# Kernel optimization log

Measured on AMD Instinct MI355X. Metric: run time of the kernel, lower is better.

The kernel has to match this reference:

```python
import jax, jax.numpy as jnp
import numpy as np

LN_EPS = 1e-12  # BERT LayerNorm eps


def _layernorm(x, g, b):
    mu = jnp.mean(x, axis=-1, keepdims=True)
    var = jnp.mean(jnp.square(x - mu), axis=-1, keepdims=True)
    return (x - mu) * jax.lax.rsqrt(var + LN_EPS) * g + b


def setup_inputs() -> dict:
    key = jax.random.key(0)
    B, M, D, H, dh, R, Ro, Rf, F = 4, 2048, 768, 12, 64, 32, 256, 256, 3072
    ks = iter(jax.random.split(key, 32))
    n = lambda shape, s=0.02: jax.random.normal(next(ks), shape, jnp.float32) * s
    return {
        'x': jax.random.normal(next(ks), (B, M, D), jnp.float32),
        'mask': jnp.zeros((B, M), jnp.float32),  # HF-style additive mask
        'Pq': n((H, D, R)), 'Vq': n((H, R, dh)), 'bq': n((1, H, 1, dh)),
        'Pk': n((H, D, R)), 'Vk': n((H, R, dh)), 'bk': n((1, H, 1, dh)),
        'Pv': n((H, D, R)), 'Vv': n((H, R, dh)), 'bv': n((1, H, 1, dh)),
        'Uo': n((D, Ro)), 'Vo': n((Ro, D)), 'bo_attn': jnp.zeros((D,), jnp.float32),
        'U1': n((D, Rf)), 'V1': n((Rf, F)), 'b1': jnp.zeros((F,), jnp.float32),
        'U2': n((F, Rf)), 'V2': n((Rf, D)), 'b2': jnp.zeros((D,), jnp.float32),
        'ln1_g': jnp.ones((D,), jnp.float32), 'ln1_b': jnp.zeros((D,), jnp.float32),
        'ln2_g': jnp.ones((D,), jnp.float32), 'ln2_b': jnp.zeros((D,), jnp.float32),
    }


def reference(x, mask, Pq, Vq, bq, Pk, Vk, bk, Pv, Vv, bv,
              Uo, Vo, bo_attn, U1, V1, b1, U2, V2, b2,
              ln1_g, ln1_b, ln2_g, ln2_b):
    B, M, D = x.shape
    H, dh = Pq.shape[0], Vq.shape[2]
    # low-rank per-head Q/K/V: x @ P (bhmr) then @ V (bhmd) + bias
    q = jnp.einsum('bhmr,hrd->bhmd', jnp.einsum('bmd,hdr->bhmr', x, Pq), Vq) + bq
    k = jnp.einsum('bhmr,hrd->bhmd', jnp.einsum('bmd,hdr->bhmr', x, Pk), Vk) + bk
    v = jnp.einsum('bhmr,hrd->bhmd', jnp.einsum('bmd,hdr->bhmr', x, Pv), Vv) + bv
    # attention (flash_svd_attention math: scaled dot-product + additive mask)
    scores = jnp.einsum('bhmd,bhnd->bhmn', q, k) / jnp.sqrt(jnp.float32(dh))
    scores = scores + mask[:, None, None, :]
    attn = jnp.einsum('bhmn,bhnd->bhmd', jax.nn.softmax(scores, axis=-1), v)
    attn = attn.transpose(0, 2, 1, 3).reshape(B, M, D)
    # low-rank output projection + residual + LN1
    x1 = _layernorm(x + (attn @ Uo) @ Vo + bo_attn, ln1_g, ln1_b)
    # low-rank FFN (BERT intermediate: exact GELU)
    mid = x1 @ U1
    y = (jax.nn.gelu(mid @ V1 + b1, approximate=False) @ U2) @ V2 + b2
    return _layernorm(x1 + y, ln2_g, ln2_b)
```

## Files before the change

### kernel.cpp

```cpp
#include <hip/hip_runtime.h>
#include <hip/hip_bf16.h>
#include <math.h>

typedef __hip_bfloat16 bf16;
typedef __attribute__((ext_vector_type(8))) short short8;
typedef __attribute__((ext_vector_type(4))) short short4v;
typedef __attribute__((ext_vector_type(4))) float f32x4;

__device__ __forceinline__ float to_f(float x) { return x; }
__device__ __forceinline__ float to_f(bf16 x) { return __bfloat162float(x); }

template <typename T> __device__ __forceinline__ T from_f(float x);
template <> __device__ __forceinline__ float from_f<float>(float x) { return x; }
template <> __device__ __forceinline__ bf16 from_f<bf16>(float x) { return __float2bfloat16(x); }

__device__ __forceinline__ float gelu_exact(float x) {
    return 0.5f * x * (1.0f + erff(x * 0.70710678118654752f));
}

#define GLD_LDS16(g, l)                                               \
    __builtin_amdgcn_global_load_lds(                                 \
        (const __attribute__((address_space(1))) void*)(g),           \
        (__attribute__((address_space(3))) void*)(l), 16, 0, 0)

__global__ __launch_bounds__(256) void build_w_qkv_lds(const float* __restrict__ Pq,
                                                       const float* __restrict__ Vq,
                                                       const float* __restrict__ Pk,
                                                       const float* __restrict__ Vk,
                                                       const float* __restrict__ Pv,
                                                       const float* __restrict__ Vv,
                                                       bf16* __restrict__ Wt) {
    const int dt = blockIdx.x;
    const int h = blockIdx.y;
    const int which = blockIdx.z;
    const float* P = (which == 0) ? Pq : (which == 1) ? Pk : Pv;
    const float* V = (which == 0) ? Vq : (which == 1) ? Vk : Vv;
    __shared__ __align__(16) float Ps[128][36];
    __shared__ __align__(16) float Vs[32][64];
    __shared__ __align__(16) unsigned int Ot[64][68];
    const int tid = threadIdx.x;

    const float* pbase = P + ((size_t)h * 768 + dt * 128) * 32;
#pragma unroll
    for (int i = 0; i < 4; i++) {
        int idx = tid + i * 256;
        float4 v4 = ((const float4*)pbase)[idx];
        *(float4*)&Ps[idx >> 3][(idx & 7) * 4] = v4;
    }
    const float* vbase = V + (size_t)h * 2048;
#pragma unroll
    for (int i = 0; i < 2; i++) {
        int idx = tid + i * 256;
        ((float4*)&Vs[0][0])[idx] = ((const float4*)vbase)[idx];
    }
    __syncthreads();

    const int e = tid & 63, w = tid >> 6;
    float vreg[32];
#pragma unroll
    for (int r = 0; r < 32; r++) vreg[r] = Vs[r][e];

#pragma unroll
    for (int dp = 0; dp < 16; dp++) {
        const int d0 = w * 32 + dp * 2;
        float a0 = 0.f, a1 = 0.f;
#pragma unroll
        for (int r4 = 0; r4 < 8; r4++) {
            float4 p0 = *(const float4*)&Ps[d0][r4 * 4];
            float4 p1 = *(const float4*)&Ps[d0 + 1][r4 * 4];
            a0 += p0.x * vreg[r4 * 4] + p0.y * vreg[r4 * 4 + 1] + p0.z * vreg[r4 * 4 + 2] + p0.w * vreg[r4 * 4 + 3];
            a1 += p1.x * vreg[r4 * 4] + p1.y * vreg[r4 * 4 + 1] + p1.z * vreg[r4 * 4 + 2] + p1.w * vreg[r4 * 4 + 3];
        }
        unsigned int lo = (unsigned int)(unsigned short)__builtin_bit_cast(short, from_f<bf16>(a0));
        unsigned int hi = (unsigned int)(unsigned short)__builtin_bit_cast(short, from_f<bf16>(a1));
        Ot[e][w * 16 + dp] = lo | (hi << 16);
    }
    __syncthreads();

    const int erow = tid >> 2, c0 = (tid & 3) * 16;
    bf16* dst = Wt + ((size_t)which * 768 + h * 64 + erow) * 768 + dt * 128 + c0 * 2;
    uint4 u0 = *(const uint4*)&Ot[erow][c0];
    uint4 u1 = *(const uint4*)&Ot[erow][c0 + 4];
    uint4 u2 = *(const uint4*)&Ot[erow][c0 + 8];
    uint4 u3 = *(const uint4*)&Ot[erow][c0 + 12];
    *(uint4*)(dst) = u0;
    *(uint4*)(dst + 8) = u1;
    *(uint4*)(dst + 16) = u2;
    *(uint4*)(dst + 24) = u3;
}

__global__ __launch_bounds__(256) void cast_transpose_t(const float* __restrict__ in,
                                                        bf16* __restrict__ out,
                                                        int R, int Cc) {
    __shared__ float t[32][33];
    const int r0 = blockIdx.x * 32, c0 = blockIdx.y * 32;
    const int tx = threadIdx.x & 31, ty = threadIdx.x >> 5;
#pragma unroll
    for (int i = 0; i < 4; i++)
        t[ty + i * 8][tx] = in[(size_t)(r0 + ty + i * 8) * Cc + c0 + tx];
    __syncthreads();
#pragma unroll
    for (int i = 0; i < 4; i++)
        out[(size_t)(c0 + ty + i * 8) * R + r0 + tx] = from_f<bf16>(t[tx][ty + i * 8]);
}

__global__ __launch_bounds__(256) void cast_f32_bf16(const float* __restrict__ in,
                                                     bf16* __restrict__ out, int n4) {
    int t = blockIdx.x * 256 + threadIdx.x;
    if (t >= n4) return;
    float4 v = ((const float4*)in)[t];
    bf16 tmp[4] = {from_f<bf16>(v.x), from_f<bf16>(v.y), from_f<bf16>(v.z), from_f<bf16>(v.w)};
    ((short4v*)out)[t] = *(short4v*)tmp;
}

__global__ __launch_bounds__(256) void pack_bias_qkv(const float* __restrict__ bq,
                                                     const float* __restrict__ bk,
                                                     const float* __restrict__ bv,
                                                     float* __restrict__ out) {
    int t = blockIdx.x * 256 + threadIdx.x;
    if (t >= 768) return;
    out[t] = bq[t];
    out[768 + t] = bk[t];
    out[1536 + t] = bv[t];
}

template <typename TOUT, int EPI>
__global__ __launch_bounds__(256) void gemm_mfma(const bf16* __restrict__ A,
                                                 const bf16* __restrict__ Bt,
                                                 const float* __restrict__ bias,
                                                 TOUT* __restrict__ C,
                                                 int M, int N, int K) {
    __shared__ __align__(16) bf16 As[128 * 32];
    __shared__ __align__(16) bf16 Bs[128 * 32];
    const int tid = threadIdx.x;
    const int w = tid >> 6, lane = tid & 63;
    const int l = lane & 15, quad = lane >> 4;
    const int wm = w >> 1, wn = w & 1;
    const int m0 = blockIdx.x * 128, n0 = blockIdx.y * 128;

    const int r_in = lane >> 2;
    const int slot = lane & 3;
    const int rA0 = 2 * w * 16 + r_in, rA1 = rA0 + 16;
    const int q0 = slot ^ ((rA0 >> 1) & 3);
    const int q1 = slot ^ ((rA1 >> 1) & 3);
    const bf16* a0 = A + (size_t)(m0 + rA0) * K + q0 * 8;
    const bf16* a1 = A + (size_t)(m0 + rA1) * K + q1 * 8;
    const bf16* b0 = Bt + (size_t)(n0 + rA0) * K + q0 * 8;
    const bf16* b1 = Bt + (size_t)(n0 + rA1) * K + q1 * 8;
    bf16* lA0 = As + 2 * w * 512;
    bf16* lA1 = lA0 + 512;
    bf16* lB0 = Bs + 2 * w * 512;
    bf16* lB1 = lB0 + 512;

    const int swz = (quad ^ ((l >> 1) & 3)) * 8;
    f32x4 acc[4][4] = {};

    for (int k0 = 0; k0 < K; k0 += 32) {
        GLD_LDS16(a0 + k0, lA0);
        GLD_LDS16(a1 + k0, lA1);
        GLD_LDS16(b0 + k0, lB0);
        GLD_LDS16(b1 + k0, lB1);
        __syncthreads();
        short8 af[4], bfr[4];
#pragma unroll
        for (int mt = 0; mt < 4; mt++)
            af[mt] = *(const short8*)&As[(wm * 64 + mt * 16 + l) * 32 + swz];
#pragma unroll
        for (int nt = 0; nt < 4; nt++)
            bfr[nt] = *(const short8*)&Bs[(wn * 64 + nt * 16 + l) * 32 + swz];
#pragma unroll
        for (int mt = 0; mt < 4; mt++)
#pragma unroll
            for (int nt = 0; nt < 4; nt++)
                acc[mt][nt] = __builtin_amdgcn_mfma_f32_16x16x32_bf16(af[mt], bfr[nt], acc[mt][nt], 0, 0, 0);
        __syncthreads();
    }

    float bs[4];
#pragma unroll
    for (int nt = 0; nt < 4; nt++)
        bs[nt] = bias ? bias[n0 + wn * 64 + nt * 16 + l] : 0.f;
#pragma unroll
    for (int mt = 0; mt < 4; mt++) {
#pragma unroll
        for (int nt = 0; nt < 4; nt++) {
            const int col = n0 + wn * 64 + nt * 16 + l;
#pragma unroll
            for (int r = 0; r < 4; r++) {
                const int row = m0 + wm * 64 + mt * 16 + quad * 4 + r;
                float val = acc[mt][nt][r] + bs[nt];
                if (EPI == 1) val = gelu_exact(val);
                C[(size_t)row * N + col] = from_f<TOUT>(val);
            }
        }
    }
}

__global__ __launch_bounds__(256) void transpose_v(const bf16* __restrict__ qkv,
                                                   bf16* __restrict__ vt) {
    __shared__ __align__(16) bf16 t[64][72];
    const int m0 = blockIdx.x * 64;
    const int h = blockIdx.y;
    const int tid = threadIdx.x;
    const int r = tid >> 2, c0 = (tid & 3) * 16;
    {
        const size_t g = (size_t)(m0 + r) * 2304 + 1536 + h * 64 + c0;
        *(short8*)&t[r][c0] = *(const short8*)(qkv + g);
        *(short8*)&t[r][c0 + 8] = *(const short8*)(qkv + g + 8);
    }
    __syncthreads();
    const int b = m0 >> 11, mm = m0 & 2047;
    const int e = tid >> 2, mi0 = (tid & 3) * 16;
    bf16 tmp[16];
#pragma unroll
    for (int j = 0; j < 16; j++) tmp[j] = t[mi0 + j][e];
    bf16* dst = vt + (((size_t)b * 12 + h) * 64 + e) * 2048 + mm + mi0;
    *(short8*)dst = *(short8*)&tmp[0];
    *(short8*)(dst + 8) = *(short8*)&tmp[8];
}

__global__ __launch_bounds__(256, 2) void flash_attn_mfma(const bf16* __restrict__ qkv,
                                                          const bf16* __restrict__ vt,
                                                          const float* __restrict__ mask,
                                                          bf16* __restrict__ attn) {
    const int qt = blockIdx.x, h = blockIdx.y, b = blockIdx.z;
    const int tid = threadIdx.x;
    const int w = tid >> 6, lane = tid & 63;
    const int l = lane & 15, quad = lane >> 4;

    __shared__ __align__(16) bf16 Ks[64 * 64];
    __shared__ __align__(16) bf16 Vs[64 * 64];
    __shared__ __align__(16) bf16 Ps[4][16 * 64];
    __shared__ float msk2[64];

    const float C1 = 0.125f * 1.44269504088896f;

    short8 qf[2][2];
#pragma unroll
    for (int mt = 0; mt < 2; mt++) {
        const int qrow = qt * 128 + w * 32 + mt * 16 + l;
        const bf16* qp = qkv + ((size_t)b * 2048 + qrow) * 2304 + h * 64 + quad * 8;
        qf[mt][0] = *(const short8*)qp;
        qf[mt][1] = *(const short8*)(qp + 32);
    }

    f32x4 of[2][4] = {};
    float lsum[2] = {0.f, 0.f};

    for (int kc = 0; kc < 2048; kc += 64) {
        __syncthreads();
#pragma unroll
        for (int i = 0; i < 2; i++) {
            const int cid = (w * 2 + i) * 64 + lane;
            const int row = cid >> 3, slot = cid & 7;
            const int gq = slot ^ (row & 7);
            const bf16* kp = qkv + ((size_t)b * 2048 + kc + row) * 2304 + 768 + h * 64 + gq * 8;
            GLD_LDS16(kp, &Ks[(size_t)cid * 8]);
            const bf16* vp = vt + (((size_t)b * 12 + h) * 64 + row) * 2048 + kc + gq * 8;
            GLD_LDS16(vp, &Vs[(size_t)cid * 8]);
        }
        if (tid < 64) msk2[tid] = mask[(size_t)b * 2048 + kc + tid] * 1.44269504088896f;
        __syncthreads();

        f32x4 st[2][4];
#pragma unroll
        for (int nt = 0; nt < 4; nt++) {
            const int rb = (nt * 16 + l) * 64;
            short8 kf0 = *(const short8*)&Ks[rb + ((quad) ^ (l & 7)) * 8];
            short8 kf1 = *(const short8*)&Ks[rb + ((4 + quad) ^ (l & 7)) * 8];
#pragma unroll
            for (int mt = 0; mt < 2; mt++) {
                f32x4 a = {};
                a = __builtin_amdgcn_mfma_f32_16x16x32_bf16(kf0, qf[mt][0], a, 0, 0, 0);
                a = __builtin_amdgcn_mfma_f32_16x16x32_bf16(kf1, qf[mt][1], a, 0, 0, 0);
                st[mt][nt] = a;
            }
        }

        float mk[4][4];
#pragma unroll
        for (int nt = 0; nt < 4; nt++)
#pragma unroll
            for (int r = 0; r < 4; r++) mk[nt][r] = msk2[nt * 16 + quad * 4 + r];

#pragma unroll
        for (int mt = 0; mt < 2; mt++) {
#pragma unroll
            for (int nt = 0; nt < 4; nt++) {
                short4v ps;
#pragma unroll
                for (int r = 0; r < 4; r++) {
                    float p = exp2f(fmaf(st[mt][nt][r], C1, mk[nt][r]));
                    lsum[mt] += p;
                    ps[r] = __builtin_bit_cast(short, from_f<bf16>(p));
                }
                const int slot8 = (2 * nt + (quad >> 1)) ^ (l & 7);
                *(short4v*)&Ps[w][mt * 0 + l * 64 + slot8 * 8 + (quad & 1) * 4] = ps;
            }
            short8 pa0 = *(const short8*)&Ps[w][l * 64 + ((quad) ^ (l & 7)) * 8];
            short8 pa1 = *(const short8*)&Ps[w][l * 64 + ((4 + quad) ^ (l & 7)) * 8];
#pragma unroll
            for (int nt = 0; nt < 4; nt++) {
                const int rb = (nt * 16 + l) * 64;
                short8 vf0 = *(const short8*)&Vs[rb + ((quad) ^ (l & 7)) * 8];
                short8 vf1 = *(const short8*)&Vs[rb + ((4 + quad) ^ (l & 7)) * 8];
                of[mt][nt] = __builtin_amdgcn_mfma_f32_16x16x32_bf16(pa0, vf0, of[mt][nt], 0, 0, 0);
                of[mt][nt] = __builtin_amdgcn_mfma_f32_16x16x32_bf16(pa1, vf1, of[mt][nt], 0, 0, 0);
            }
        }
    }

#pragma unroll
    for (int mt = 0; mt < 2; mt++) {
        lsum[mt] += __shfl_xor(lsum[mt], 16, 64);
        lsum[mt] += __shfl_xor(lsum[mt], 32, 64);
        lsum[mt] = 1.f / lsum[mt];
    }
#pragma unroll
    for (int mt = 0; mt < 2; mt++) {
#pragma unroll
        for (int r = 0; r < 4; r++) {
            const float iv = __shfl(lsum[mt], (lane & 48) | (quad * 4 + r), 64);
            const int row = qt * 128 + w * 32 + mt * 16 + quad * 4 + r;
#pragma unroll
            for (int nt = 0; nt < 4; nt++)
                attn[((size_t)b * 2048 + row) * 768 + h * 64 + nt * 16 + l] =
                    from_f<bf16>(of[mt][nt][r] * iv);
        }
    }
}

template <typename TIN, typename TOUT>
__global__ __launch_bounds__(256) void ln_kernel(const TIN* __restrict__ base,
                                                 const float* __restrict__ add,
                                                 const float* __restrict__ gamma,
                                                 const float* __restrict__ beta,
                                                 TOUT* __restrict__ out) {
    const int row = blockIdx.x;
    const int tid = threadIdx.x;
    __shared__ float red[4];
    const size_t o = (size_t)row * 768;
    float v[3];
#pragma unroll
    for (int i = 0; i < 3; i++) {
        int d = tid + i * 256;
        v[i] = to_f(base[o + d]) + add[o + d];
    }
    float s = v[0] + v[1] + v[2];
#pragma unroll
    for (int off = 32; off > 0; off >>= 1) s += __shfl_down(s, off, 64);
    const int wave = tid >> 6, lane = tid & 63;
    if (lane == 0) red[wave] = s;
    __syncthreads();
    float mu = (red[0] + red[1] + red[2] + red[3]) * (1.0f / 768.0f);
    float d0 = v[0] - mu, d1 = v[1] - mu, d2 = v[2] - mu;
    float sq = d0 * d0 + d1 * d1 + d2 * d2;
    __syncthreads();
#pragma unroll
    for (int off = 32; off > 0; off >>= 1) sq += __shfl_down(sq, off, 64);
    if (lane == 0) red[wave] = sq;
    __syncthreads();
    float var = (red[0] + red[1] + red[2] + red[3]) * (1.0f / 768.0f);
    float rs = rsqrtf(var + 1e-12f);
#pragma unroll
    for (int i = 0; i < 3; i++) {
        int d = tid + i * 256;
        float y = (v[i] - mu) * rs * gamma[d] + beta[d];
        out[o + d] = from_f<TOUT>(y);
    }
}

extern "C" void kernel_launch(void* const* d_in, const int* in_sizes, int n_in,
                              void* d_out, int out_size, void* d_ws, size_t ws_size,
                              hipStream_t stream) {
    const float* x    = (const float*)d_in[0];
    const float* mask = (const float*)d_in[1];
    const float* Pq = (const float*)d_in[2];
    const float* Vq = (const float*)d_in[3];
    const float* bq = (const float*)d_in[4];
    const float* Pk = (const float*)d_in[5];
    const float* Vk = (const float*)d_in[6];
    const float* bk = (const float*)d_in[7];
    const float* Pv = (const float*)d_in[8];
    const float* Vv = (const float*)d_in[9];
    const float* bv = (const float*)d_in[10];
    const float* Uo = (const float*)d_in[11];
    const float* Vo = (const float*)d_in[12];
    const float* bo = (const float*)d_in[13];
    const float* U1 = (const float*)d_in[14];
    const float* V1 = (const float*)d_in[15];
    const float* b1 = (const float*)d_in[16];
    const float* U2 = (const float*)d_in[17];
    const float* V2 = (const float*)d_in[18];
    const float* b2 = (const float*)d_in[19];
    const float* g1 = (const float*)d_in[20];
    const float* be1 = (const float*)d_in[21];
    const float* g2 = (const float*)d_in[22];
    const float* be2 = (const float*)d_in[23];

    char* p = (char*)d_ws;
    bf16* Wqkv_t = (bf16*)p;            p += (size_t)2304 * 768 * 2;
    bf16* Wo_t   = (bf16*)p;            p += (size_t)768 * 768 * 2;
    bf16* U1t    = (bf16*)p;            p += (size_t)256 * 768 * 2;
    bf16* V1t    = (bf16*)p;            p += (size_t)3072 * 256 * 2;
    bf16* U2t    = (bf16*)p;            p += (size_t)256 * 3072 * 2;
    bf16* V2t    = (bf16*)p;            p += (size_t)768 * 256 * 2;
    float* bias_qkv = (float*)p;        p += (size_t)2304 * 4;
    bf16* xb     = (bf16*)p;
    bf16* x1b    = xb;                  p += (size_t)8192 * 768 * 2;
    bf16* qkv    = (bf16*)p;
    bf16* gbuf   = qkv;                 p += (size_t)8192 * 2304 * 2;
    bf16* vtb    = (bf16*)p;            p += (size_t)8192 * 768 * 2;
    bf16* attnb  = (bf16*)p;
    bf16* t2     = attnb;               p += (size_t)8192 * 768 * 2;
    float* bufA  = (float*)p;           p += (size_t)8192 * 768 * 4;
    bf16* t1     = (bf16*)p;            p += (size_t)8192 * 256 * 2;
    bf16* Vot = (bf16*)bufA;
    bf16* Uob = Vot + (size_t)768 * 256;

    build_w_qkv_lds<<<dim3(6, 12, 3), 256, 0, stream>>>(Pq, Vq, Pk, Vk, Pv, Vv, Wqkv_t);
    cast_transpose_t<<<dim3(8, 24), 256, 0, stream>>>(Vo, Vot, 256, 768);
    cast_f32_bf16<<<192, 256, 0, stream>>>(Uo, Uob, 768 * 256 / 4);
    gemm_mfma<bf16, 0><<<dim3(6, 6), 256, 0, stream>>>(Vot, Uob, nullptr, Wo_t, 768, 768, 256);
    cast_transpose_t<<<dim3(24, 8), 256, 0, stream>>>(U1, U1t, 768, 256);
    cast_transpose_t<<<dim3(8, 96), 256, 0, stream>>>(V1, V1t, 256, 3072);
    cast_transpose_t<<<dim3(96, 8), 256, 0, stream>>>(U2, U2t, 3072, 256);
    cast_transpose_t<<<dim3(8, 24), 256, 0, stream>>>(V2, V2t, 256, 768);
    pack_bias_qkv<<<3, 256, 0, stream>>>(bq, bk, bv, bias_qkv);
    cast_f32_bf16<<<6144, 256, 0, stream>>>(x, xb, 8192 * 768 / 4);

    gemm_mfma<bf16, 0><<<dim3(64, 18), 256, 0, stream>>>(xb, Wqkv_t, bias_qkv, qkv, 8192, 2304, 768);

    transpose_v<<<dim3(128, 12), 256, 0, stream>>>(qkv, vtb);

    flash_attn_mfma<<<dim3(16, 12, 4), 256, 0, stream>>>(qkv, vtb, mask, attnb);

    gemm_mfma<float, 0><<<dim3(64, 6), 256, 0, stream>>>(attnb, Wo_t, bo, bufA, 8192, 768, 768);

    ln_kernel<float, bf16><<<8192, 256, 0, stream>>>(x, bufA, g1, be1, x1b);

    gemm_mfma<bf16, 0><<<dim3(64, 2), 256, 0, stream>>>(x1b, U1t, nullptr, t1, 8192, 256, 768);

    gemm_mfma<bf16, 1><<<dim3(64, 24), 256, 0, stream>>>(t1, V1t, b1, gbuf, 8192, 3072, 256);

    gemm_mfma<bf16, 0><<<dim3(64, 2), 256, 0, stream>>>(gbuf, U2t, nullptr, t2, 8192, 256, 3072);

    gemm_mfma<float, 0><<<dim3(64, 6), 256, 0, stream>>>(t2, V2t, b2, bufA, 8192, 768, 256);

    ln_kernel<bf16, float><<<8192, 256, 0, stream>>>(x1b, bufA, g2, be2, (float*)d_out);
}
```

Baseline: 484.9 us.

## Switch flash attention to 32x32x16 MFMA with two 64-row waves per block

Rewrites the attention kernel to use 32x32x16 bf16 MFMA tiles instead of 16x16x32, with each of two waves owning 64 query rows (block shrinks from 256 to 128 threads). This doubles per-wave work, increasing reuse of K/V fragments loaded from LDS and cutting LDS reads per MFMA. The trade-offs are higher register pressure from the larger accumulators, fewer waves per block to hide latency, and a softmax normaliser that now round-trips through shared memory. A small cosmetic cleanup in build_w_qkv_lds is also included.

```diff
diff --git a/kernel.cpp b/kernel.cpp
--- a/kernel.cpp
+++ b/kernel.cpp
@@ -6,6 +6,7 @@
 typedef __attribute__((ext_vector_type(8))) short short8;
 typedef __attribute__((ext_vector_type(4))) short short4v;
 typedef __attribute__((ext_vector_type(4))) float f32x4;
+typedef __attribute__((ext_vector_type(16))) float f32x16;
 
 __device__ __forceinline__ float to_f(float x) { return x; }
 __device__ __forceinline__ float to_f(bf16 x) { return __bfloat162float(x); }
@@ -79,14 +80,10 @@
 
     const int erow = tid >> 2, c0 = (tid & 3) * 16;
     bf16* dst = Wt + ((size_t)which * 768 + h * 64 + erow) * 768 + dt * 128 + c0 * 2;
-    uint4 u0 = *(const uint4*)&Ot[erow][c0];
-    uint4 u1 = *(const uint4*)&Ot[erow][c0 + 4];
-    uint4 u2 = *(const uint4*)&Ot[erow][c0 + 8];
-    uint4 u3 = *(const uint4*)&Ot[erow][c0 + 12];
-    *(uint4*)(dst) = u0;
-    *(uint4*)(dst + 8) = u1;
-    *(uint4*)(dst + 16) = u2;
-    *(uint4*)(dst + 24) = u3;
+    *(uint4*)(dst) = *(const uint4*)&Ot[erow][c0];
+    *(uint4*)(dst + 8) = *(const uint4*)&Ot[erow][c0 + 4];
+    *(uint4*)(dst + 16) = *(const uint4*)&Ot[erow][c0 + 8];
+    *(uint4*)(dst + 24) = *(const uint4*)&Ot[erow][c0 + 12];
 }
 
 __global__ __launch_bounds__(256) void cast_transpose_t(const float* __restrict__ in,
@@ -219,39 +216,40 @@
     *(short8*)(dst + 8) = *(short8*)&tmp[8];
 }
 
-__global__ __launch_bounds__(256, 2) void flash_attn_mfma(const bf16* __restrict__ qkv,
+__global__ __launch_bounds__(128, 2) void flash_attn_mfma(const bf16* __restrict__ qkv,
                                                           const bf16* __restrict__ vt,
                                                           const float* __restrict__ mask,
                                                           bf16* __restrict__ attn) {
     const int qt = blockIdx.x, h = blockIdx.y, b = blockIdx.z;
     const int tid = threadIdx.x;
     const int w = tid >> 6, lane = tid & 63;
-    const int l = lane & 15, quad = lane >> 4;
+    const int l31 = lane & 31, hl = lane >> 5;
 
     __shared__ __align__(16) bf16 Ks[64 * 64];
     __shared__ __align__(16) bf16 Vs[64 * 64];
-    __shared__ __align__(16) bf16 Ps[4][16 * 64];
-    __shared__ float msk2[64];
+    __shared__ __align__(16) bf16 Ps[2][64 * 64];
+    __shared__ __align__(16) float msk2[64];
+    __shared__ float lsq[128];
 
     const float C1 = 0.125f * 1.44269504088896f;
 
-    short8 qf[2][2];
-#pragma unroll
-    for (int mt = 0; mt < 2; mt++) {
-        const int qrow = qt * 128 + w * 32 + mt * 16 + l;
-        const bf16* qp = qkv + ((size_t)b * 2048 + qrow) * 2304 + h * 64 + quad * 8;
-        qf[mt][0] = *(const short8*)qp;
-        qf[mt][1] = *(const short8*)(qp + 32);
-    }
-
-    f32x4 of[2][4] = {};
+    short8 qf[2][4];
+#pragma unroll
+    for (int nq = 0; nq < 2; nq++) {
+        const int qrow = qt * 128 + w * 64 + nq * 32 + l31;
+        const bf16* qp = qkv + ((size_t)b * 2048 + qrow) * 2304 + h * 64 + 8 * hl;
+#pragma unroll
+        for (int dep = 0; dep < 4; dep++) qf[nq][dep] = *(const short8*)(qp + dep * 16);
+    }
+
+    f32x16 of[2][2] = {};
     float lsum[2] = {0.f, 0.f};
 
     for (int kc = 0; kc < 2048; kc += 64) {
         __syncthreads();
 #pragma unroll
-        for (int i = 0; i < 2; i++) {
-            const int cid = (w * 2 + i) * 64 + lane;
+        for (int i = 0; i < 4; i++) {
+            const int cid = i * 128 + tid;
             const int row = cid >> 3, slot = cid & 7;
             const int gq = slot ^ (row & 7);
             const bf16* kp = qkv + ((size_t)b * 2048 + kc + row) * 2304 + 768 + h * 64 + gq * 8;
@@ -262,70 +260,97 @@
         if (tid < 64) msk2[tid] = mask[(size_t)b * 2048 + kc + tid] * 1.44269504088896f;
         __syncthreads();
 
-        f32x4 st[2][4];
-#pragma unroll
-        for (int nt = 0; nt < 4; nt++) {
-            const int rb = (nt * 16 + l) * 64;
-            short8 kf0 = *(const short8*)&Ks[rb + ((quad) ^ (l & 7)) * 8];
-            short8 kf1 = *(const short8*)&Ks[rb + ((4 + quad) ^ (l & 7)) * 8];
-#pragma unroll
-            for (int mt = 0; mt < 2; mt++) {
-                f32x4 a = {};
-                a = __builtin_amdgcn_mfma_f32_16x16x32_bf16(kf0, qf[mt][0], a, 0, 0, 0);
-                a = __builtin_amdgcn_mfma_f32_16x16x32_bf16(kf1, qf[mt][1], a, 0, 0, 0);
-                st[mt][nt] = a;
-            }
-        }
-
-        float mk[4][4];
-#pragma unroll
-        for (int nt = 0; nt < 4; nt++)
-#pragma unroll
-            for (int r = 0; r < 4; r++) mk[nt][r] = msk2[nt * 16 + quad * 4 + r];
-
-#pragma unroll
-        for (int mt = 0; mt < 2; mt++) {
-#pragma unroll
-            for (int nt = 0; nt < 4; nt++) {
-                short4v ps;
-#pragma unroll
-                for (int r = 0; r < 4; r++) {
-                    float p = exp2f(fmaf(st[mt][nt][r], C1, mk[nt][r]));
-                    lsum[mt] += p;
-                    ps[r] = __builtin_bit_cast(short, from_f<bf16>(p));
+        f32x16 st[2][2] = {};
+#pragma unroll
+        for (int kt = 0; kt < 2; kt++) {
+            const int krow = kt * 32 + l31;
+#pragma unroll
+            for (int dep = 0; dep < 4; dep++) {
+                const int phys = (dep * 2 + hl) ^ (krow & 7);
+                short8 kf = *(const short8*)&Ks[krow * 64 + phys * 8];
+#pragma unroll
+                for (int nq = 0; nq < 2; nq++)
+                    st[kt][nq] = __builtin_amdgcn_mfma_f32_32x32x16_bf16(kf, qf[nq][dep], st[kt][nq], 0, 0, 0);
+            }
+        }
+
+        float4 mrow[2][4];
+#pragma unroll
+        for (int kt = 0; kt < 2; kt++)
+#pragma unroll
+            for (int g = 0; g < 4; g++)
+                mrow[kt][g] = *(const float4*)&msk2[kt * 32 + g * 8 + 4 * hl];
+
+#pragma unroll
+        for (int nq = 0; nq < 2; nq++) {
+            const int q = nq * 32 + l31;
+#pragma unroll
+            for (int kt = 0; kt < 2; kt++) {
+#pragma unroll
+                for (int g = 0; g < 4; g++) {
+                    const float* mg = (const float*)&mrow[kt][g];
+                    short4v ps;
+#pragma unroll
+                    for (int r = 0; r < 4; r++) {
+                        float p = exp2f(fmaf(st[kt][nq][g * 4 + r], C1, mg[r]));
+                        lsum[nq] += p;
+                        ps[r] = __builtin_bit_cast(short, from_f<bf16>(p));
+                    }
+                    const int chunk = kt * 4 + g;
+                    const int phys = chunk ^ (q & 7);
+                    *(short4v*)&Ps[w][q * 64 + phys * 8 + 4 * hl] = ps;
                 }
-                const int slot8 = (2 * nt + (quad >> 1)) ^ (l & 7);
-                *(short4v*)&Ps[w][mt * 0 + l * 64 + slot8 * 8 + (quad & 1) * 4] = ps;
-            }
-            short8 pa0 = *(const short8*)&Ps[w][l * 64 + ((quad) ^ (l & 7)) * 8];
-            short8 pa1 = *(const short8*)&Ps[w][l * 64 + ((4 + quad) ^ (l & 7)) * 8];
-#pragma unroll
-            for (int nt = 0; nt < 4; nt++) {
-                const int rb = (nt * 16 + l) * 64;
-                short8 vf0 = *(const short8*)&Vs[rb + ((quad) ^ (l & 7)) * 8];
-                short8 vf1 = *(const short8*)&Vs[rb + ((4 + quad) ^ (l & 7)) * 8];
-                of[mt][nt] = __builtin_amdgcn_mfma_f32_16x16x32_bf16(pa0, vf0, of[mt][nt], 0, 0, 0);
-                of[mt][nt] = __builtin_amdgcn_mfma_f32_16x16x32_bf16(pa1, vf1, of[mt][nt], 0, 0, 0);
-            }
-        }
-    }
-
-#pragma unroll
-    for (int mt = 0; mt < 2; mt++) {
-        lsum[mt] += __shfl_xor(lsum[mt], 16, 64);
-        lsum[mt] += __shfl_xor(lsum[mt], 32, 64);
-        lsum[mt] = 1.f / lsum[mt];
-    }
-#pragma unroll
-    for (int mt = 0; mt < 2; mt++) {
-#pragma unroll
-        for (int r = 0; r < 4; r++) {
-            const float iv = __shfl(lsum[mt], (lane & 48) | (quad * 4 + r), 64);
-            const int row = qt * 128 + w * 32 + mt * 16 + quad * 4 + r;
-#pragma unroll
-            for (int nt = 0; nt < 4; nt++)
-                attn[((size_t)b * 2048 + row) * 768 + h * 64 + nt * 16 + l] =
-                    from_f<bf16>(of[mt][nt][r] * iv);
+            }
+        }
+
+        short8 vf[2][4];
+#pragma unroll
+        for (int ntd = 0; ntd < 2; ntd++) {
+            const int drow = ntd * 32 + l31;
+#pragma unroll
+            for (int dep = 0; dep < 4; dep++) {
+                const int phys = (dep * 2 + hl) ^ (drow & 7);
+                vf[ntd][dep] = *(const short8*)&Vs[drow * 64 + phys * 8];
+            }
+        }
+
+#pragma unroll
+        for (int mtq = 0; mtq < 2; mtq++) {
+            const int q = mtq * 32 + l31;
+            short8 pa[4];
+#pragma unroll
+            for (int dep = 0; dep < 4; dep++) {
+                const int phys = (dep * 2 + hl) ^ (q & 7);
+                pa[dep] = *(const short8*)&Ps[w][q * 64 + phys * 8];
+            }
+#pragma unroll
+            for (int ntd = 0; ntd < 2; ntd++)
+#pragma unroll
+                for (int dep = 0; dep < 4; dep++)
+                    of[mtq][ntd] = __builtin_amdgcn_mfma_f32_32x32x16_bf16(pa[dep], vf[ntd][dep], of[mtq][ntd], 0, 0, 0);
+        }
+    }
+
+#pragma unroll
+    for (int nq = 0; nq < 2; nq++) {
+        lsum[nq] += __shfl_xor(lsum[nq], 32, 64);
+        if (hl == 0) lsq[w * 64 + nq * 32 + l31] = 1.f / lsum[nq];
+    }
+
+#pragma unroll
+    for (int mtq = 0; mtq < 2; mtq++) {
+#pragma unroll
+        for (int g = 0; g < 4; g++) {
+#pragma unroll
+            for (int r = 0; r < 4; r++) {
+                const int qloc = mtq * 32 + g * 8 + 4 * hl + r;
+                const float iv = lsq[w * 64 + qloc];
+                const int row = qt * 128 + w * 64 + qloc;
+#pragma unroll
+                for (int ntd = 0; ntd < 2; ntd++)
+                    attn[((size_t)b * 2048 + row) * 768 + h * 64 + ntd * 32 + l31] =
+                        from_f<bf16>(of[mtq][ntd][g * 4 + r] * iv);
+            }
         }
     }
 }
@@ -433,7 +458,7 @@
 
     transpose_v<<<dim3(128, 12), 256, 0, stream>>>(qkv, vtb);
 
-    flash_attn_mfma<<<dim3(16, 12, 4), 256, 0, stream>>>(qkv, vtb, mask, attnb);
+    flash_attn_mfma<<<dim3(16, 12, 4), 128, 0, stream>>>(qkv, vtb, mask, attnb);
 
     gemm_mfma<float, 0><<<dim3(64, 6), 256, 0, stream>>>(attnb, Wo_t, bo, bufA, 8192, 768, 768);
 
```

New measurement: 556.4 us. 14.8% more time.

## Split attention over key halves and add a combine kernel

Applied to the files above, without the earlier changes.

Splits each attention block's key range into two halves (split-K), doubling the grid to 1536 blocks. Each half writes an unnormalized bf16 partial output and row sums, and a new combine kernel adds the halves and normalizes. Other changes raise the launch-bounds occupancy hint to 4, load the mask straight from global memory instead of staging it in LDS, and reorder the PV MFMA loop so V fragments are reused across both M tiles. The cost is an extra kernel launch and extra global traffic for the partial outputs, plus a little precision loss from storing unnormalized partials in bf16.

```diff
diff --git a/kernel.cpp b/kernel.cpp
--- a/kernel.cpp
+++ b/kernel.cpp
@@ -79,14 +79,10 @@
 
     const int erow = tid >> 2, c0 = (tid & 3) * 16;
     bf16* dst = Wt + ((size_t)which * 768 + h * 64 + erow) * 768 + dt * 128 + c0 * 2;
-    uint4 u0 = *(const uint4*)&Ot[erow][c0];
-    uint4 u1 = *(const uint4*)&Ot[erow][c0 + 4];
-    uint4 u2 = *(const uint4*)&Ot[erow][c0 + 8];
-    uint4 u3 = *(const uint4*)&Ot[erow][c0 + 12];
-    *(uint4*)(dst) = u0;
-    *(uint4*)(dst + 8) = u1;
-    *(uint4*)(dst + 16) = u2;
-    *(uint4*)(dst + 24) = u3;
+    *(uint4*)(dst) = *(const uint4*)&Ot[erow][c0];
+    *(uint4*)(dst + 8) = *(const uint4*)&Ot[erow][c0 + 4];
+    *(uint4*)(dst + 16) = *(const uint4*)&Ot[erow][c0 + 8];
+    *(uint4*)(dst + 24) = *(const uint4*)&Ot[erow][c0 + 12];
 }
 
 __global__ __launch_bounds__(256) void cast_transpose_t(const float* __restrict__ in,
@@ -219,21 +215,24 @@
     *(short8*)(dst + 8) = *(short8*)&tmp[8];
 }
 
-__global__ __launch_bounds__(256, 2) void flash_attn_mfma(const bf16* __restrict__ qkv,
+__global__ __launch_bounds__(256, 4) void flash_attn_mfma(const bf16* __restrict__ qkv,
                                                           const bf16* __restrict__ vt,
                                                           const float* __restrict__ mask,
-                                                          bf16* __restrict__ attn) {
-    const int qt = blockIdx.x, h = blockIdx.y, b = blockIdx.z;
+                                                          bf16* __restrict__ opart0,
+                                                          bf16* __restrict__ opart1,
+                                                          float* __restrict__ lpart) {
+    const int qt = blockIdx.x, h = blockIdx.y;
+    const int b = blockIdx.z >> 1, kh = blockIdx.z & 1;
     const int tid = threadIdx.x;
     const int w = tid >> 6, lane = tid & 63;
     const int l = lane & 15, quad = lane >> 4;
 
     __shared__ __align__(16) bf16 Ks[64 * 64];
     __shared__ __align__(16) bf16 Vs[64 * 64];
-    __shared__ __align__(16) bf16 Ps[4][16 * 64];
-    __shared__ float msk2[64];
+    __shared__ __align__(16) bf16 Ps[4 * 32 * 64];
 
     const float C1 = 0.125f * 1.44269504088896f;
+    const float LOG2E = 1.44269504088896f;
 
     short8 qf[2][2];
 #pragma unroll
@@ -246,8 +245,10 @@
 
     f32x4 of[2][4] = {};
     float lsum[2] = {0.f, 0.f};
-
-    for (int kc = 0; kc < 2048; kc += 64) {
+    bf16* Pw = Ps + w * 2048;
+
+    const int kc_end = kh * 1024 + 1024;
+    for (int kc = kh * 1024; kc < kc_end; kc += 64) {
         __syncthreads();
 #pragma unroll
         for (int i = 0; i < 2; i++) {
@@ -259,7 +260,10 @@
             const bf16* vp = vt + (((size_t)b * 12 + h) * 64 + row) * 2048 + kc + gq * 8;
             GLD_LDS16(vp, &Vs[(size_t)cid * 8]);
         }
-        if (tid < 64) msk2[tid] = mask[(size_t)b * 2048 + kc + tid] * 1.44269504088896f;
+        float4 mrow[4];
+#pragma unroll
+        for (int nt = 0; nt < 4; nt++)
+            mrow[nt] = *(const float4*)&mask[(size_t)b * 2048 + kc + nt * 16 + quad * 4];
         __syncthreads();
 
         f32x4 st[2][4];
@@ -277,11 +281,13 @@
             }
         }
 
-        float mk[4][4];
-#pragma unroll
-        for (int nt = 0; nt < 4; nt++)
-#pragma unroll
-            for (int r = 0; r < 4; r++) mk[nt][r] = msk2[nt * 16 + quad * 4 + r];
+        float mkl[4][4];
+#pragma unroll
+        for (int nt = 0; nt < 4; nt++) {
+            const float* mg = (const float*)&mrow[nt];
+#pragma unroll
+            for (int r = 0; r < 4; r++) mkl[nt][r] = mg[r] * LOG2E;
+        }
 
 #pragma unroll
         for (int mt = 0; mt < 2; mt++) {
@@ -290,22 +296,31 @@
                 short4v ps;
 #pragma unroll
                 for (int r = 0; r < 4; r++) {
-                    float p = exp2f(fmaf(st[mt][nt][r], C1, mk[nt][r]));
+                    float p = exp2f(fmaf(st[mt][nt][r], C1, mkl[nt][r]));
                     lsum[mt] += p;
                     ps[r] = __builtin_bit_cast(short, from_f<bf16>(p));
                 }
                 const int slot8 = (2 * nt + (quad >> 1)) ^ (l & 7);
-                *(short4v*)&Ps[w][mt * 0 + l * 64 + slot8 * 8 + (quad & 1) * 4] = ps;
+                *(short4v*)&Pw[(mt * 16 + l) * 64 + slot8 * 8 + (quad & 1) * 4] = ps;
             }
-            short8 pa0 = *(const short8*)&Ps[w][l * 64 + ((quad) ^ (l & 7)) * 8];
-            short8 pa1 = *(const short8*)&Ps[w][l * 64 + ((4 + quad) ^ (l & 7)) * 8];
-#pragma unroll
-            for (int nt = 0; nt < 4; nt++) {
-                const int rb = (nt * 16 + l) * 64;
-                short8 vf0 = *(const short8*)&Vs[rb + ((quad) ^ (l & 7)) * 8];
-                short8 vf1 = *(const short8*)&Vs[rb + ((4 + quad) ^ (l & 7)) * 8];
-                of[mt][nt] = __builtin_amdgcn_mfma_f32_16x16x32_bf16(pa0, vf0, of[mt][nt], 0, 0, 0);
-                of[mt][nt] = __builtin_amdgcn_mfma_f32_16x16x32_bf16(pa1, vf1, of[mt][nt], 0, 0, 0);
+        }
+
+        short8 pa[2][2];
+#pragma unroll
+        for (int mt = 0; mt < 2; mt++)
+#pragma unroll
+            for (int ks = 0; ks < 2; ks++)
+                pa[mt][ks] = *(const short8*)&Pw[(mt * 16 + l) * 64 + ((ks * 4 + quad) ^ (l & 7)) * 8];
+
+#pragma unroll
+        for (int nt = 0; nt < 4; nt++) {
+            const int rb = (nt * 16 + l) * 64;
+            short8 vf0 = *(const short8*)&Vs[rb + ((quad) ^ (l & 7)) * 8];
+            short8 vf1 = *(const short8*)&Vs[rb + ((4 + quad) ^ (l & 7)) * 8];
+#pragma unroll
+            for (int mt = 0; mt < 2; mt++) {
+                of[mt][nt] = __builtin_amdgcn_mfma_f32_16x16x32_bf16(pa[mt][0], vf0, of[mt][nt], 0, 0, 0);
+                of[mt][nt] = __builtin_amdgcn_mfma_f32_16x16x32_bf16(pa[mt][1], vf1, of[mt][nt], 0, 0, 0);
             }
         }
     }
@@ -314,20 +329,45 @@
     for (int mt = 0; mt < 2; mt++) {
         lsum[mt] += __shfl_xor(lsum[mt], 16, 64);
         lsum[mt] += __shfl_xor(lsum[mt], 32, 64);
-        lsum[mt] = 1.f / lsum[mt];
-    }
+        if (lane < 16)
+            lpart[(((size_t)kh * 4 + b) * 12 + h) * 2048 + qt * 128 + w * 32 + mt * 16 + lane] = lsum[mt];
+    }
+
+    bf16* op = kh ? opart1 : opart0;
 #pragma unroll
     for (int mt = 0; mt < 2; mt++) {
 #pragma unroll
         for (int r = 0; r < 4; r++) {
-            const float iv = __shfl(lsum[mt], (lane & 48) | (quad * 4 + r), 64);
             const int row = qt * 128 + w * 32 + mt * 16 + quad * 4 + r;
 #pragma unroll
             for (int nt = 0; nt < 4; nt++)
-                attn[((size_t)b * 2048 + row) * 768 + h * 64 + nt * 16 + l] =
-                    from_f<bf16>(of[mt][nt][r] * iv);
-        }
-    }
+                op[((size_t)b * 2048 + row) * 768 + h * 64 + nt * 16 + l] =
+                    from_f<bf16>(of[mt][nt][r]);
+        }
+    }
+}
+
+__global__ __launch_bounds__(256) void attn_combine(const bf16* __restrict__ o0,
+                                                    const bf16* __restrict__ o1,
+                                                    const float* __restrict__ lp,
+                                                    bf16* __restrict__ outp) {
+    const int t = blockIdx.x * 256 + threadIdx.x;
+    const int col4 = t % 192;
+    const int row = t / 192;
+    const int b = row >> 11, m = row & 2047;
+    const int h = col4 >> 4;
+    const float l0 = lp[((size_t)b * 12 + h) * 2048 + m];
+    const float l1 = lp[((size_t)(4 + b) * 12 + h) * 2048 + m];
+    const float iv = 1.f / (l0 + l1);
+    short4v a = ((const short4v*)o0)[t];
+    short4v c = ((const short4v*)o1)[t];
+    bf16 r[4];
+#pragma unroll
+    for (int i = 0; i < 4; i++) {
+        float f = to_f(__builtin_bit_cast(bf16, a[i])) + to_f(__builtin_bit_cast(bf16, c[i]));
+        r[i] = from_f<bf16>(f * iv);
+    }
+    ((short4v*)outp)[t] = *(short4v*)r;
 }
 
 template <typename TIN, typename TOUT>
@@ -417,6 +457,8 @@
     bf16* t1     = (bf16*)p;            p += (size_t)8192 * 256 * 2;
     bf16* Vot = (bf16*)bufA;
     bf16* Uob = Vot + (size_t)768 * 256;
+    bf16* opart1 = (bf16*)bufA;
+    float* lpart = (float*)((char*)bufA + (size_t)8192 * 768 * 2);
 
     build_w_qkv_lds<<<dim3(6, 12, 3), 256, 0, stream>>>(Pq, Vq, Pk, Vk, Pv, Vv, Wqkv_t);
     cast_transpose_t<<<dim3(8, 24), 256, 0, stream>>>(Vo, Vot, 256, 768);
@@ -433,7 +475,8 @@
 
     transpose_v<<<dim3(128, 12), 256, 0, stream>>>(qkv, vtb);
 
-    flash_attn_mfma<<<dim3(16, 12, 4), 256, 0, stream>>>(qkv, vtb, mask, attnb);
+    flash_attn_mfma<<<dim3(16, 12, 8), 256, 0, stream>>>(qkv, vtb, mask, attnb, opart1, lpart);
+    attn_combine<<<6144, 256, 0, stream>>>(attnb, opart1, lpart, attnb);
 
     gemm_mfma<float, 0><<<dim3(64, 6), 256, 0, stream>>>(attnb, Wo_t, bo, bufA, 8192, 768, 768);
 
```

New measurement: 511.0 us. +5.4%, slower.
